# Kernel optimization log

Hardware: AMD Instinct MI355X
Metric: run time of the kernel (lower is better)

The kernel has to match this reference:

```python
import jax, jax.numpy as jnp
import numpy as np

B, GH, GW = 8, 32, 32
S = GH * GW            # 1024
HIDDEN = 512
D = 64                 # head_dim
NUM_HOPS = 2
EPS = 1e-6


def setup_inputs() -> dict:
    key = jax.random.key(0)
    ks = jax.random.split(key, 8)

    def init(k, shape, std):
        return (jax.random.normal(k, shape) * std).astype(jnp.float32)

    x = jax.random.normal(ks[0], (B, S, HIDDEN), dtype=jnp.float32)
    Wq = init(ks[1], (D, HIDDEN), HIDDEN ** -0.5)
    Wk = init(ks[2], (D, HIDDEN), HIDDEN ** -0.5)
    Wv = init(ks[3], (D, HIDDEN), HIDDEN ** -0.5)
    bias_table = init(ks[4], (2 * GH - 1, 2 * GW - 1), 0.02)
    fusion_w = jnp.ones((NUM_HOPS, 3), dtype=jnp.float32)
    fusion_b = jnp.zeros((NUM_HOPS,), dtype=jnp.float32)
    hop_W = init(ks[5], (NUM_HOPS, D, D), D ** -0.5)
    gate_W = init(ks[6], (NUM_HOPS, HIDDEN), HIDDEN ** -0.5)
    gate_b = jnp.zeros((NUM_HOPS,), dtype=jnp.float32)
    out_W = init(ks[7], (HIDDEN, D), D ** -0.5)
    temperature = jnp.ones((1,), dtype=jnp.float32)

    # relative position index [S, S] (buffer, constant)
    coords = np.stack(np.meshgrid(np.arange(GH), np.arange(GW), indexing='ij')).reshape(2, -1)
    rel = coords[:, :, None] - coords[:, None, :]
    rel[0] += GH - 1
    rel[1] += GW - 1
    rel_idx = jnp.asarray(rel[0] * (2 * GW - 1) + rel[1], dtype=jnp.int32)

    return dict(x=x, Wq=Wq, Wk=Wk, Wv=Wv, bias_table=bias_table,
                fusion_w=fusion_w, fusion_b=fusion_b, hop_W=hop_W,
                gate_W=gate_W, gate_b=gate_b, out_W=out_W,
                temperature=temperature, rel_idx=rel_idx)


def _rotate_half(u):
    d = u.shape[-1] // 2
    return jnp.concatenate([-u[..., d:], u[..., :d]], axis=-1)


def _prob_log(p):
    p = jnp.clip(p, EPS, 1.0 - EPS)
    return jnp.log(p / (1.0 - p + EPS))


def _mat_exp(M, h):
    R = M
    for _ in range(h - 1):
        R = jnp.matmul(R, M)
    return R


def _row_norm(M):
    return M / (jnp.sum(M, axis=-1, keepdims=True) + EPS)


def reference(x, Wq, Wk, Wv, bias_table, fusion_w, fusion_b, hop_W,
              gate_W, gate_b, out_W, temperature, rel_idx):
    b, s, hdim = x.shape
    d = Wq.shape[0]
    n_hops = hop_W.shape[0]
    scale = jnp.sqrt(jnp.float32(d))

    Q = jnp.einsum('bsh,dh->bsd', x, Wq)
    K = jnp.einsum('bsh,dh->bsd', x, Wk)
    V = jnp.einsum('bsh,dh->bsd', x, Wv)

    # RoPE (cached cos/sin are deterministic functions of S, D)
    inv_freq = 1.0 / (10000.0 ** (jnp.arange(0, d, 2, dtype=jnp.float32) / d))
    t = jnp.arange(s, dtype=jnp.float32)
    emb = jnp.concatenate([jnp.outer(t, inv_freq)] * 2, axis=-1)  # [S, D]
    cos, sin = jnp.cos(emb), jnp.sin(emb)
    Q = Q * cos + _rotate_half(Q) * sin
    K = K * cos + _rotate_half(K) * sin

    pb = bias_table.reshape(-1)[rel_idx]  # [S, S]
    scores = (jnp.einsum('bsd,btd->bst', Q, K) / scale + pb[None])
    scores = scores / jnp.clip(temperature, 0.1, None)
    A = jax.nn.softmax(scores, axis=-1)  # [B, S, S]

    A_T = jnp.swapaxes(A, -1, -2)
    AAt = jnp.matmul(A, A_T)
    AtA = jnp.matmul(A_T, A)

    hop_outs = []
    for hop in range(n_hops):
        h = hop + 1
        A_seq = _row_norm(_mat_exp(A, h))
        A_co = _row_norm(_mat_exp(AAt, h))
        A_sp = _row_norm(_mat_exp(AtA, h))
        fused_logit = (fusion_b[hop]
                       + fusion_w[hop, 0] * _prob_log(A_seq)
                       + fusion_w[hop, 1] * _prob_log(A_co)
                       + fusion_w[hop, 2] * _prob_log(A_sp))
        fused = _row_norm(jax.nn.sigmoid(fused_logit))
        hop_v = jnp.einsum('bsd,ed->bse', V, hop_W[hop])
        hop_outs.append(jnp.matmul(fused, hop_v))  # [B, S, D]

    gate = jax.nn.softmax(jnp.einsum('bsh,gh->bsg', x, gate_W) + gate_b, axis=-1)
    combined = sum(hop_outs[i] * gate[..., i:i + 1] for i in range(n_hops))
    return jnp.einsum('bsd,hd->bsh', combined, out_W)
```

## Files before the change

### kernel.cpp

```cpp
#include <hip/hip_runtime.h>
#include <hip/hip_bf16.h>

#define BB 8
#define SS 1024
#define HH 512
#define DD 64

typedef unsigned short u16;
typedef short v8s __attribute__((ext_vector_type(8)));
typedef float v4f __attribute__((ext_vector_type(4)));

__device__ __forceinline__ float bf2f(u16 u) {
    union { unsigned int i; float f; } v; v.i = ((unsigned int)u) << 16; return v.f;
}
__device__ __forceinline__ u16 f2bf(float f) {
    union { float f; unsigned int i; } v; v.f = f;
    unsigned int u = v.i;
    unsigned int r = u + 0x7fffu + ((u >> 16) & 1u);
    return (u16)(r >> 16);
}

__device__ __forceinline__ void gload16(const u16* g, u16* l) {
    __builtin_amdgcn_global_load_lds(
        (const __attribute__((address_space(1))) void*)g,
        (__attribute__((address_space(3))) void*)l,
        16, 0, 0);
}

__device__ __forceinline__ void tile_1024(
    const u16* __restrict__ Xb, const u16* __restrict__ Yb,
    u16* __restrict__ Cd, int tm, int tn, u16* Xs, u16* Ys, int mirror)
{
    int t = threadIdx.x, lane = t & 63, w = t >> 6;
    int wm = (w & 1) << 6, wn = (w >> 1) << 6;
    int fr = lane & 15, q = lane >> 4, m7 = fr & 7;
    int subrow = lane >> 3, cch = (lane & 7) ^ subrow;

    const u16* xg[4]; const u16* yg[4]; u16* xl[4]; u16* yl[4];
    #pragma unroll
    for (int i = 0; i < 4; i++) {
        int r = i * 32 + w * 8 + subrow;
        xg[i] = Xb + (long)(tm + r) * 1024 + cch * 8;
        yg[i] = Yb + (long)(tn + r) * 1024 + cch * 8;
        xl[i] = Xs + (i * 32 + w * 8) * 64;
        yl[i] = Ys + (i * 32 + w * 8) * 64;
    }

    v4f acc[4][4];
    #pragma unroll
    for (int i = 0; i < 4; i++)
        #pragma unroll
        for (int j = 0; j < 4; j++) {
            acc[i][j][0] = 0.f; acc[i][j][1] = 0.f; acc[i][j][2] = 0.f; acc[i][j][3] = 0.f;
        }

    for (int k0 = 0; k0 < 1024; k0 += 64) {
        __syncthreads();
        #pragma unroll
        for (int i = 0; i < 4; i++) { gload16(xg[i] + k0, xl[i]); gload16(yg[i] + k0, yl[i]); }
        __syncthreads();
        v8s af[2][4], bfr[2][4];
        #pragma unroll
        for (int h = 0; h < 2; h++) {
            int ca = (((h << 2) + q) ^ m7) << 3;
            #pragma unroll
            for (int s = 0; s < 4; s++) {
                af[h][s]  = *(const v8s*)(Xs + (wm + s * 16 + fr) * 64 + ca);
                bfr[h][s] = *(const v8s*)(Ys + (wn + s * 16 + fr) * 64 + ca);
            }
        }
        #pragma unroll
        for (int h = 0; h < 2; h++)
            #pragma unroll
            for (int i = 0; i < 4; i++)
                #pragma unroll
                for (int j = 0; j < 4; j++)
                    acc[i][j] = __builtin_amdgcn_mfma_f32_16x16x32_bf16(af[h][i], bfr[h][j], acc[i][j], 0, 0, 0);
    }
    #pragma unroll
    for (int i = 0; i < 4; i++) {
        int rowb = tm + wm + i * 16 + q * 4;
        #pragma unroll
        for (int j = 0; j < 4; j++) {
            int col = tn + wn + j * 16 + fr;
            ushort4 pv;
            pv.x = f2bf(acc[i][j][0]); pv.y = f2bf(acc[i][j][1]);
            pv.z = f2bf(acc[i][j][2]); pv.w = f2bf(acc[i][j][3]);
            #pragma unroll
            for (int r = 0; r < 4; r++)
                Cd[(long)(rowb + r) * 1024 + col] = ((u16*)&pv)[r];
            if (mirror)
                *(ushort4*)(Cd + (long)col * 1024 + rowb) = pv;
        }
    }
}

__device__ __forceinline__ void hopv_tile(
    const u16* __restrict__ Vrows, const u16* __restrict__ Hw,
    u16* __restrict__ hopVT, int tm, u16* Xs, u16* Ys)
{
    int t = threadIdx.x, lane = t & 63, w = t >> 6;
    int wm = (w & 1) << 6, wn = (w >> 1) << 6;
    int fr = lane & 15, q = lane >> 4, m7 = fr & 7;
    int subrow = lane >> 3, cch = (lane & 7) ^ subrow;

    #pragma unroll
    for (int i = 0; i < 4; i++) {
        int r = i * 32 + w * 8 + subrow;
        gload16(Vrows + (long)(tm + r) * 64 + cch * 8, Xs + (i * 32 + w * 8) * 64);
        gload16(Hw + (long)r * 64 + cch * 8, Ys + (i * 32 + w * 8) * 64);
    }
    __syncthreads();

    v4f acc[4][4];
    #pragma unroll
    for (int i = 0; i < 4; i++)
        #pragma unroll
        for (int j = 0; j < 4; j++) {
            acc[i][j][0] = 0.f; acc[i][j][1] = 0.f; acc[i][j][2] = 0.f; acc[i][j][3] = 0.f;
        }
    v8s af[2][4], bfr[2][4];
    #pragma unroll
    for (int h = 0; h < 2; h++) {
        int ca = (((h << 2) + q) ^ m7) << 3;
        #pragma unroll
        for (int s = 0; s < 4; s++) {
            af[h][s]  = *(const v8s*)(Xs + (wm + s * 16 + fr) * 64 + ca);
            bfr[h][s] = *(const v8s*)(Ys + (wn + s * 16 + fr) * 64 + ca);
        }
    }
    #pragma unroll
    for (int h = 0; h < 2; h++)
        #pragma unroll
        for (int i = 0; i < 4; i++)
            #pragma unroll
            for (int j = 0; j < 4; j++)
                acc[i][j] = __builtin_amdgcn_mfma_f32_16x16x32_bf16(af[h][i], bfr[h][j], acc[i][j], 0, 0, 0);

    int z = tm >> 10, sb = tm & 1023;
    #pragma unroll
    for (int i = 0; i < 4; i++) {
        int rowb = wm + i * 16 + q * 4;
        #pragma unroll
        for (int j = 0; j < 4; j++) {
            int colY = wn + j * 16 + fr;
            int hop = colY >> 6, e = colY & 63;
            ushort4 pv;
            pv.x = f2bf(acc[i][j][0]); pv.y = f2bf(acc[i][j][1]);
            pv.z = f2bf(acc[i][j][2]); pv.w = f2bf(acc[i][j][3]);
            *(ushort4*)(hopVT + (long)(hop * 8 + z) * 65536 + (long)e * 1024 + sb + rowb) = pv;
        }
    }
}

__device__ __forceinline__ void hop_tile(
    const u16* __restrict__ Fb, const u16* __restrict__ Hb,
    int y, int tmt, float* __restrict__ Pd, u16* Fs, u16* Hs)
{
    int tm = tmt * 128, kb = y * 256;
    int t = threadIdx.x, lane = t & 63, w = t >> 6;
    int fr = lane & 15, q = lane >> 4, m7 = fr & 7;
    int subrow = lane >> 3, cch = (lane & 7) ^ subrow;

    const u16* fg[4]; u16* fl[4]; const u16* hg[2]; u16* hl[2];
    #pragma unroll
    for (int i = 0; i < 4; i++) {
        int r = i * 32 + w * 8 + subrow;
        fg[i] = Fb + (long)(tm + r) * 1024 + cch * 8;
        fl[i] = Fs + (i * 32 + w * 8) * 64;
    }
    #pragma unroll
    for (int i = 0; i < 2; i++) {
        int r = i * 32 + w * 8 + subrow;
        hg[i] = Hb + (long)r * 1024 + cch * 8;
        hl[i] = Hs + (i * 32 + w * 8) * 64;
    }

    v4f acc[2][4];
    #pragma unroll
    for (int i = 0; i < 2; i++)
        #pragma unroll
        for (int j = 0; j < 4; j++) {
            acc[i][j][0] = 0.f; acc[i][j][1] = 0.f; acc[i][j][2] = 0.f; acc[i][j][3] = 0.f;
        }

    for (int k0 = kb; k0 < kb + 256; k0 += 64) {
        __syncthreads();
        #pragma unroll
        for (int i = 0; i < 4; i++) gload16(fg[i] + k0, fl[i]);
        #pragma unroll
        for (int i = 0; i < 2; i++) gload16(hg[i] + k0, hl[i]);
        __syncthreads();
        v8s af[2][2], bfr[2][4];
        #pragma unroll
        for (int h = 0; h < 2; h++) {
            int ca = (((h << 2) + q) ^ m7) << 3;
            #pragma unroll
            for (int s = 0; s < 2; s++)
                af[h][s] = *(const v8s*)(Fs + (w * 32 + s * 16 + fr) * 64 + ca);
            #pragma unroll
            for (int s = 0; s < 4; s++)
                bfr[h][s] = *(const v8s*)(Hs + (s * 16 + fr) * 64 + ca);
        }
        #pragma unroll
        for (int h = 0; h < 2; h++)
            #pragma unroll
            for (int i = 0; i < 2; i++)
                #pragma unroll
                for (int j = 0; j < 4; j++)
                    acc[i][j] = __builtin_amdgcn_mfma_f32_16x16x32_bf16(af[h][i], bfr[h][j], acc[i][j], 0, 0, 0);
    }
    #pragma unroll
    for (int i = 0; i < 2; i++) {
        int rowb = tm + w * 32 + i * 16 + q * 4;
        #pragma unroll
        for (int j = 0; j < 4; j++) {
            int col = j * 16 + fr;
            #pragma unroll
            for (int r = 0; r < 4; r++)
                Pd[(long)(rowb + r) * 64 + col] = acc[i][j][r];
        }
    }
}

__device__ __forceinline__ void fused_row(
    const u16* __restrict__ r1, const u16* __restrict__ r2, const u16* __restrict__ r3,
    float w0, float w1, float w2, float b0, u16* __restrict__ Frow, int lane)
{
    int base = lane << 4;
    union U { uint4 v; u16 s[8]; };
    U a[2], b[2], c[2];
    a[0].v = *(const uint4*)(r1 + base); a[1].v = *(const uint4*)(r1 + base + 8);
    b[0].v = *(const uint4*)(r2 + base); b[1].v = *(const uint4*)(r2 + base + 8);
    c[0].v = *(const uint4*)(r3 + base); c[1].v = *(const uint4*)(r3 + base + 8);
    float m1[16], m2[16], m3[16];
    float s1 = 0.f, s2 = 0.f, s3 = 0.f;
    #pragma unroll
    for (int h = 0; h < 2; h++)
        #pragma unroll
        for (int e = 0; e < 8; e++) {
            int k = h * 8 + e;
            m1[k] = bf2f(a[h].s[e]); m2[k] = bf2f(b[h].s[e]); m3[k] = bf2f(c[h].s[e]);
            s1 += m1[k]; s2 += m2[k]; s3 += m3[k];
        }
    #pragma unroll
    for (int o = 1; o < 64; o <<= 1) {
        s1 += __shfl_xor(s1, o); s2 += __shfl_xor(s2, o); s3 += __shfl_xor(s3, o);
    }
    float i1 = 1.f / (s1 + 1e-6f), i2 = 1.f / (s2 + 1e-6f), i3 = 1.f / (s3 + 1e-6f);
    float sig[16];
    float ssum = 0.f;
    #pragma unroll
    for (int k = 0; k < 16; k++) {
        float p1 = fminf(fmaxf(m1[k] * i1, 1e-6f), 1.0f - 1e-6f);
        float p2 = fminf(fmaxf(m2[k] * i2, 1e-6f), 1.0f - 1e-6f);
        float p3 = fminf(fmaxf(m3[k] * i3, 1e-6f), 1.0f - 1e-6f);
        float l1 = __logf(p1 / (1.0f - p1 + 1e-6f));
        float l2 = __logf(p2 / (1.0f - p2 + 1e-6f));
        float l3 = __logf(p3 / (1.0f - p3 + 1e-6f));
        float lg = b0 + w0 * l1 + w1 * l2 + w2 * l3;
        float sg = 1.0f / (1.0f + __expf(-lg));
        sig[k] = sg; ssum += sg;
    }
    #pragma unroll
    for (int o = 1; o < 64; o <<= 1) ssum += __shfl_xor(ssum, o);
    float inv = 1.0f / (ssum + 1e-6f);
    U o0, o1;
    #pragma unroll
    for (int e = 0; e < 8; e++) { o0.s[e] = f2bf(sig[e] * inv); o1.s[e] = f2bf(sig[8 + e] * inv); }
    *(uint4*)(Frow + base) = o0.v;
    *(uint4*)(Frow + base + 8) = o1.v;
}

__global__ __launch_bounds__(256) void k_qksm(
    const u16* __restrict__ Qb, const u16* __restrict__ Kb,
    const float* __restrict__ btab, const float* __restrict__ temp,
    u16* __restrict__ A, u16* __restrict__ AT)
{
    __shared__ __align__(16) float smf[3969];
    __shared__ float lred[4][16];
    int t = threadIdx.x, lane = t & 63, w = t >> 6;
    int fr = lane & 15, q4 = lane >> 4;
    int bx = blockIdx.x;
    int z = bx >> 6;
    int rb = (bx & 63) << 4;
    for (int i = t; i < 3969; i += 256) smf[i] = btab[i];
    __syncthreads();
    float invt = 1.0f / fmaxf(temp[0], 0.1f);
    const long SD = (long)SS * DD;
    const long SSq = (long)SS * SS;
    const u16* qrow = Qb + (long)z * SD + (long)(rb + fr) * 64 + q4 * 8;
    v8s aq0 = *(const v8s*)(qrow);
    v8s aq1 = *(const v8s*)(qrow + 32);
    int ih[4], iw[4];
    #pragma unroll
    for (int r = 0; r < 4; r++) {
        int ii = rb + q4 * 4 + r;
        ih[r] = ii >> 5; iw[r] = ii & 31;
    }
    const u16* kb0 = Kb + (long)z * SD + q4 * 8;
    int c0 = w << 8;
    float ef[16][4];
    float l0 = 0.f, l1 = 0.f, l2 = 0.f, l3 = 0.f;
    #pragma unroll
    for (int f = 0; f < 16; f++) {
        int colK = c0 + f * 16 + fr;
        const u16* krow = kb0 + (long)colK * 64;
        v8s bk0 = *(const v8s*)(krow);
        v8s bk1 = *(const v8s*)(krow + 32);
        v4f acc = {0.f, 0.f, 0.f, 0.f};
        acc = __builtin_amdgcn_mfma_f32_16x16x32_bf16(aq0, bk0, acc, 0, 0, 0);
        acc = __builtin_amdgcn_mfma_f32_16x16x32_bf16(aq1, bk1, acc, 0, 0, 0);
        int jh = colK >> 5, jw = colK & 31;
        #pragma unroll
        for (int r = 0; r < 4; r++) {
            float pb = smf[(ih[r] - jh + 31) * 63 + (iw[r] - jw + 31)];
            float s = (acc[r] * 0.125f + pb) * invt;
            float e = __expf(s);
            ef[f][r] = e;
            if (r == 0) l0 += e; else if (r == 1) l1 += e;
            else if (r == 2) l2 += e; else l3 += e;
        }
    }
    #pragma unroll
    for (int o = 1; o < 16; o <<= 1) {
        l0 += __shfl_xor(l0, o); l1 += __shfl_xor(l1, o);
        l2 += __shfl_xor(l2, o); l3 += __shfl_xor(l3, o);
    }
    if (fr == 0) {
        lred[w][q4 * 4 + 0] = l0; lred[w][q4 * 4 + 1] = l1;
        lred[w][q4 * 4 + 2] = l2; lred[w][q4 * 4 + 3] = l3;
    }
    __syncthreads();
    float invl[4];
    #pragma unroll
    for (int r = 0; r < 4; r++) {
        int idx = q4 * 4 + r;
        invl[r] = 1.0f / (lred[0][idx] + lred[1][idx] + lred[2][idx] + lred[3][idx]);
    }
    u16* Ab = A + (long)z * SSq;
    u16* ATb = AT + (long)z * SSq;
    #pragma unroll
    for (int f = 0; f < 16; f++) {
        int colK = c0 + f * 16 + fr;
        ushort4 pv;
        u16* pp = (u16*)&pv;
        #pragma unroll
        for (int r = 0; r < 4; r++) {
            u16 bv = f2bf(ef[f][r] * invl[r]);
            pp[r] = bv;
            Ab[(long)(rb + q4 * 4 + r) * 1024 + colK] = bv;
        }
        *(ushort4*)(ATb + (long)colK * 1024 + rb + q4 * 4) = pv;
    }
}

__global__ __launch_bounds__(256) void gemm_link1(
    const u16* __restrict__ A, const u16* __restrict__ AT,
    u16* __restrict__ AAt, u16* __restrict__ AtA, u16* __restrict__ A2,
    const u16* __restrict__ Vb, const u16* __restrict__ hopWb,
    u16* __restrict__ hopVT)
{
    __shared__ u16 Xs[128 * 64];
    __shared__ u16 Ys[128 * 64];
    const long SSq = (long)SS * SS;
    if (blockIdx.x >= 1088) {
        hopv_tile(Vb, hopWb, hopVT, (blockIdx.x - 1088) * 128, Xs, Ys);
        return;
    }
    int b = blockIdx.x & 7;
    int job = blockIdx.x >> 3;
    const u16* Xb; const u16* Yb; u16* Cd;
    int ti, tj, mir;
    if (job < 72) {
        int tt = job < 36 ? job : job - 36;
        ti = 0;
        while (tt >= 8 - ti) { tt -= 8 - ti; ti++; }
        tj = ti + tt;
        mir = (ti != tj);
        if (job < 36) { Xb = A  + b * SSq; Yb = Xb; Cd = AAt + b * SSq; }
        else          { Xb = AT + b * SSq; Yb = Xb; Cd = AtA + b * SSq; }
    } else {
        int jj = job - 72;
        ti = jj >> 3; tj = jj & 7; mir = 0;
        Xb = A + b * SSq; Yb = AT + b * SSq; Cd = A2 + b * SSq;
    }
    tile_1024(Xb, Yb, Cd, ti * 128, tj * 128, Xs, Ys, mir);
}

__global__ __launch_bounds__(256) void k_link2_fused0(
    const u16* __restrict__ AAt, const u16* __restrict__ AtA,
    u16* __restrict__ AAt2, u16* __restrict__ AtA2,
    const u16* __restrict__ A, const float* __restrict__ fw,
    const float* __restrict__ fbv, u16* __restrict__ F0)
{
    __shared__ u16 Xs[128 * 64];
    __shared__ u16 Ys[128 * 64];
    const long SSq = (long)SS * SS;
    int bx = blockIdx.x;
    if (bx < 576) {
        int z = bx & 15;
        int tt = bx >> 4, ti = 0;
        while (tt >= 8 - ti) { tt -= 8 - ti; ti++; }
        int tj = ti + tt;
        const u16* Xb = (z < 8 ? AAt : AtA) + (long)(z & 7) * SSq;
        u16* Cd = (z < 8 ? AAt2 : AtA2) + (long)(z & 7) * SSq;
        tile_1024(Xb, Xb, Cd, ti * 128, tj * 128, Xs, Ys, ti != tj);
    } else {
        int lane = threadIdx.x & 63, w = threadIdx.x >> 6;
        float w0 = fw[0], w1 = fw[1], w2 = fw[2], b0 = fbv[0];
        long row = (long)(bx - 576) * 4 + w;
        fused_row(A + row * 1024, AAt + row * 1024, AtA + row * 1024,
                  w0, w1, w2, b0, F0 + row * 1024, lane);
    }
}

__global__ __launch_bounds__(256) void k_hop0_fused1(
    const u16* __restrict__ F0, const u16* __restrict__ hopVT,
    float* __restrict__ Pa, float* __restrict__ Pb,
    const u16* __restrict__ A2, const u16* __restrict__ AAt2,
    const u16* __restrict__ AtA2, const float* __restrict__ fw,
    const float* __restrict__ fbv, u16* __restrict__ F1)
{
    __shared__ u16 Fs[128 * 64];
    __shared__ u16 Hs[64 * 64];
    const long SSq = (long)SS * SS;
    int bx = blockIdx.x;
    if (bx < 256) {
        int y = bx >> 6, rest = bx & 63;
        int tmt = rest >> 3, b = rest & 7;
        float* Pd = (y < 2 ? Pa + (long)y * 16 * 65536 : Pb + (long)(y - 2) * 16 * 65536)
                    + (long)b * 65536;
        hop_tile(F0 + (long)b * SSq, hopVT + (long)b * 65536, y, tmt, Pd, Fs, Hs);
    } else {
        int lane = threadIdx.x & 63, w = threadIdx.x >> 6;
        float w0 = fw[3], w1 = fw[4], w2 = fw[5], b0 = fbv[1];
        long row = (long)(bx - 256) * 4 + w;
        fused_row(A2 + row * 1024, AAt2 + row * 1024, AtA2 + row * 1024,
                  w0, w1, w2, b0, F1 + row * 1024, lane);
    }
}

__global__ __launch_bounds__(256) void gemm_hop1(
    const u16* __restrict__ F1, const u16* __restrict__ hopVT,
    float* __restrict__ Pa, float* __restrict__ Pb)
{
    __shared__ u16 Fs[128 * 64];
    __shared__ u16 Hs[64 * 64];
    const long SSq = (long)SS * SS;
    int j = blockIdx.x;
    int y = j >> 6, rest = j & 63;
    int tmt = rest >> 3, b = rest & 7;
    float* Pd = (y < 2 ? Pa + (long)y * 16 * 65536 : Pb + (long)(y - 2) * 16 * 65536)
                + (long)(8 + b) * 65536;
    hop_tile(F1 + (long)b * SSq, hopVT + (long)(8 + b) * 65536, y, tmt, Pd, Fs, Hs);
}

__global__ __launch_bounds__(256) void gemm_nt(
    const u16* __restrict__ X, long sx,
    const u16* __restrict__ Y, long sy,
    void* __restrict__ Cv, long sc,
    int M, int N, int K, int cf32)
{
    __shared__ u16 Xs[128 * 64];
    __shared__ u16 Ys[128 * 64];
    const u16* Xb = X + (long)blockIdx.z * sx;
    const u16* Yb = Y + (long)blockIdx.z * sy;
    int tm = blockIdx.x * 128, tn = blockIdx.y * 128;
    int t = threadIdx.x, lane = t & 63, w = t >> 6;
    int wm = (w & 1) << 6, wn = (w >> 1) << 6;
    int fr = lane & 15, q = lane >> 4, m7 = fr & 7;
    int subrow = lane >> 3, cch = (lane & 7) ^ subrow;

    const u16* xg[4]; const u16* yg[4]; u16* xl[4]; u16* yl[4];
    #pragma unroll
    for (int i = 0; i < 4; i++) {
        int r = i * 32 + w * 8 + subrow;
        xg[i] = Xb + (long)(tm + r) * K + cch * 8;
        yg[i] = Yb + (long)(tn + r) * K + cch * 8;
        xl[i] = Xs + (i * 32 + w * 8) * 64;
        yl[i] = Ys + (i * 32 + w * 8) * 64;
    }

    v4f acc[4][4];
    #pragma unroll
    for (int i = 0; i < 4; i++)
        #pragma unroll
        for (int j = 0; j < 4; j++) {
            acc[i][j][0] = 0.f; acc[i][j][1] = 0.f; acc[i][j][2] = 0.f; acc[i][j][3] = 0.f;
        }

    for (int k0 = 0; k0 < K; k0 += 64) {
        __syncthreads();
        #pragma unroll
        for (int i = 0; i < 4; i++) { gload16(xg[i] + k0, xl[i]); gload16(yg[i] + k0, yl[i]); }
        __syncthreads();
        v8s af[2][4], bfr[2][4];
        #pragma unroll
        for (int h = 0; h < 2; h++) {
            int ca = (((h << 2) + q) ^ m7) << 3;
            #pragma unroll
            for (int s = 0; s < 4; s++) {
                af[h][s]  = *(const v8s*)(Xs + (wm + s * 16 + fr) * 64 + ca);
                bfr[h][s] = *(const v8s*)(Ys + (wn + s * 16 + fr) * 64 + ca);
            }
        }
        #pragma unroll
        for (int h = 0; h < 2; h++)
            #pragma unroll
            for (int i = 0; i < 4; i++)
                #pragma unroll
                for (int j = 0; j < 4; j++)
                    acc[i][j] = __builtin_amdgcn_mfma_f32_16x16x32_bf16(af[h][i], bfr[h][j], acc[i][j], 0, 0, 0);
    }
    long cb = (long)blockIdx.z * sc;
    #pragma unroll
    for (int i = 0; i < 4; i++) {
        int rowb = tm + wm + i * 16 + q * 4;
        #pragma unroll
        for (int j = 0; j < 4; j++) {
            int col = tn + wn + j * 16 + fr;
            #pragma unroll
            for (int r = 0; r < 4; r++) {
                long o = cb + (long)(rowb + r) * N + col;
                if (cf32) ((float*)Cv)[o] = acc[i][j][r];
                else      ((u16*)Cv)[o] = f2bf(acc[i][j][r]);
            }
        }
    }
}

__global__ __launch_bounds__(256) void k_proj_rope(
    const u16* __restrict__ xb, const u16* __restrict__ wpack,
    const float* __restrict__ gateb, const float2* __restrict__ ropetab,
    u16* __restrict__ Qb, u16* __restrict__ Kb, u16* __restrict__ Vb,
    float* __restrict__ gate)
{
    __shared__ u16 Xs[128 * 64];
    __shared__ u16 Ys[128 * 64];
    int tm = blockIdx.x * 128, tn = blockIdx.y * 128;
    int t = threadIdx.x, lane = t & 63, w = t >> 6;
    int wm = (w & 1) << 6, wn = (w >> 1) << 6;
    int fr = lane & 15, q = lane >> 4, m7 = fr & 7;
    int subrow = lane >> 3, cch = (lane & 7) ^ subrow;

    const u16* xg[4]; const u16* yg[4]; u16* xl[4]; u16* yl[4];
    #pragma unroll
    for (int i = 0; i < 4; i++) {
        int r = i * 32 + w * 8 + subrow;
        xg[i] = xb + (long)(tm + r) * 512 + cch * 8;
        yg[i] = wpack + (long)(tn + r) * 512 + cch * 8;
        xl[i] = Xs + (i * 32 + w * 8) * 64;
        yl[i] = Ys + (i * 32 + w * 8) * 64;
    }

    v4f acc[4][4];
    #pragma unroll
    for (int i = 0; i < 4; i++)
        #pragma unroll
        for (int j = 0; j < 4; j++) {
            acc[i][j][0] = 0.f; acc[i][j][1] = 0.f; acc[i][j][2] = 0.f; acc[i][j][3] = 0.f;
        }

    for (int k0 = 0; k0 < 512; k0 += 64) {
        __syncthreads();
        #pragma unroll
        for (int i = 0; i < 4; i++) { gload16(xg[i] + k0, xl[i]); gload16(yg[i] + k0, yl[i]); }
        __syncthreads();
        v8s af[2][4], bfr[2][4];
        #pragma unroll
        for (int h = 0; h < 2; h++) {
            int ca = (((h << 2) + q) ^ m7) << 3;
            #pragma unroll
            for (int s = 0; s < 4; s++) {
                af[h][s]  = *(const v8s*)(Xs + (wm + s * 16 + fr) * 64 + ca);
                bfr[h][s] = *(const v8s*)(Ys + (wn + s * 16 + fr) * 64 + ca);
            }
        }
        #pragma unroll
        for (int h = 0; h < 2; h++)
            #pragma unroll
            for (int i = 0; i < 4; i++)
                #pragma unroll
                for (int j = 0; j < 4; j++)
                    acc[i][j] = __builtin_amdgcn_mfma_f32_16x16x32_bf16(af[h][i], bfr[h][j], acc[i][j], 0, 0, 0);
    }

    if (blockIdx.y == 0) {
        u16* dst = wn ? Kb : Qb;
        #pragma unroll
        for (int i = 0; i < 4; i++) {
            #pragma unroll
            for (int r = 0; r < 4; r++) {
                int row = tm + wm + i * 16 + q * 4 + r;
                int spos = row & (SS - 1);
                float2 t0 = ropetab[spos * 32 + fr];
                float2 t1 = ropetab[spos * 32 + 16 + fr];
                #pragma unroll
                for (int j = 0; j < 4; j++) {
                    float v = acc[i][j][r], p = acc[i][j ^ 2][r];
                    float cs = (j & 1) ? t1.x : t0.x;
                    float sn = (j & 1) ? t1.y : t0.y;
                    float o = (j & 2) ? (v * cs + p * sn) : (v * cs - p * sn);
                    dst[(long)row * 64 + j * 16 + fr] = f2bf(o);
                }
            }
        }
    } else if (wn == 0) {
        #pragma unroll
        for (int i = 0; i < 4; i++)
            #pragma unroll
            for (int j = 0; j < 4; j++)
                #pragma unroll
                for (int r = 0; r < 4; r++) {
                    int row = tm + wm + i * 16 + q * 4 + r;
                    Vb[(long)row * 64 + j * 16 + fr] = f2bf(acc[i][j][r]);
                }
    } else {
        float gb = gateb[fr & 1];
        #pragma unroll
        for (int i = 0; i < 4; i++)
            #pragma unroll
            for (int r = 0; r < 4; r++) {
                int row = tm + wm + i * 16 + q * 4 + r;
                float g = acc[i][0][r] + gb;
                float go = __shfl_xor(g, 1);
                float m = fmaxf(g, go);
                float e = __expf(g - m), eo = __expf(go - m);
                if (fr < 2) gate[(long)row * 2 + fr] = e / (e + eo);
            }
    }
}

__global__ __launch_bounds__(256) void k_pack(
    const float* __restrict__ x, const float* __restrict__ Wq,
    const float* __restrict__ Wk, const float* __restrict__ Wv,
    const float* __restrict__ gW, const float* __restrict__ hopW,
    const float* __restrict__ outW, u16* __restrict__ xb,
    u16* __restrict__ wpack, u16* __restrict__ hopWb, u16* __restrict__ outWb,
    float2* __restrict__ ropetab)
{
    int bx = blockIdx.x;
    if (bx < 4096) {
        long i = (long)bx * 256 + threadIdx.x;
        float4 v = ((const float4*)x)[i];
        ushort4 o;
        o.x = f2bf(v.x); o.y = f2bf(v.y); o.z = f2bf(v.z); o.w = f2bf(v.w);
        ((ushort4*)xb)[i] = o;
    } else if (bx < 4768) {
        int idx = (bx - 4096) * 256 + threadIdx.x;
        if (idx < 131072) {
            int r = idx >> 9, c = idx & 511;
            float v = 0.f;
            if (r < 64)       v = Wq[r * 512 + c];
            else if (r < 128) v = Wk[(r - 64) * 512 + c];
            else if (r < 192) v = Wv[(r - 128) * 512 + c];
            else if (r < 194) v = gW[(r - 192) * 512 + c];
            wpack[idx] = f2bf(v);
        } else if (idx < 131072 + 8192) {
            int i = idx - 131072;
            hopWb[i] = f2bf(hopW[i]);
        } else if (idx < 131072 + 8192 + 32768) {
            int i = idx - 131072 - 8192;
            outWb[i] = f2bf(outW[i]);
        }
    } else {
        int idx = (bx - 4768) * 256 + threadIdx.x;
        int spos = idx >> 5, f = idx & 31;
        float ang = (float)spos * exp2f(-(float)f * (13.287712379549449f / 32.0f));
        float sn, cs;
        sincosf(ang, &sn, &cs);
        ropetab[idx] = make_float2(cs, sn);
    }
}

__global__ __launch_bounds__(256) void k_combine(
    const float* __restrict__ Pa, const float* __restrict__ Pb,
    const float* __restrict__ gate, u16* __restrict__ comb)
{
    long idx = (long)blockIdx.x * 256 + threadIdx.x;
    long srow = idx >> 6;
    int b = (int)(srow >> 10);
    long o = (long)(srow & 1023) * 64 + (idx & 63);
    float h0 = Pa[(long)b * 65536 + o] + Pa[(long)(16 + b) * 65536 + o]
             + Pb[(long)b * 65536 + o] + Pb[(long)(16 + b) * 65536 + o];
    float h1 = Pa[(long)(8 + b) * 65536 + o] + Pa[(long)(24 + b) * 65536 + o]
             + Pb[(long)(8 + b) * 65536 + o] + Pb[(long)(24 + b) * 65536 + o];
    float g0 = gate[srow * 2], g1 = gate[srow * 2 + 1];
    comb[idx] = f2bf(h0 * g0 + h1 * g1);
}

extern "C" void kernel_launch(void* const* d_in, const int* in_sizes, int n_in,
                              void* d_out, int out_size, void* d_ws, size_t ws_size,
                              hipStream_t stream) {
    const float* x    = (const float*)d_in[0];
    const float* Wq   = (const float*)d_in[1];
    const float* Wk   = (const float*)d_in[2];
    const float* Wv   = (const float*)d_in[3];
    const float* btab = (const float*)d_in[4];
    const float* fw   = (const float*)d_in[5];
    const float* fbv  = (const float*)d_in[6];
    const float* hopW = (const float*)d_in[7];
    const float* gW   = (const float*)d_in[8];
    const float* gb   = (const float*)d_in[9];
    const float* outW = (const float*)d_in[10];
    const float* temp = (const float*)d_in[11];
    float* out = (float*)d_out;

    char* wsb = (char*)d_ws;
    size_t off = 0;
    auto take = [&](size_t n) { char* p = wsb + off; off += (n + 255) & ~(size_t)255; return p; };
    u16* Qb      = (u16*)take(8192L * 64 * 2);
    u16* Kb      = (u16*)take(8192L * 64 * 2);
    u16* Vb      = (u16*)take(8192L * 64 * 2);
    float* gate  = (float*)take(8192L * 2 * 4);
    u16* wpack   = (u16*)take(256L * 512 * 2);
    u16* hopWb   = (u16*)take(2L * 64 * 64 * 2);
    u16* outWb   = (u16*)take(512L * 64 * 2);
    float2* ropetab = (float2*)take(1024L * 32 * 8);
    u16* hopVT   = (u16*)take(2L * 8 * 64 * 1024 * 2);
    float* Pa    = (float*)take(2L * 16 * 65536 * 4);
    u16* comb    = (u16*)take(8192L * 64 * 2);
    char* fregion = take(8L * 1024 * 1024 * 4);
    u16* F0      = (u16*)fregion;
    u16* F1      = (u16*)fregion + 8L * 1024 * 1024;
    u16* A       = (u16*)take(8L * 1024 * 1024 * 2);
    u16* xb      = (u16*)A;
    u16* AT      = (u16*)take(8L * 1024 * 1024 * 2);
    float* Pb    = (float*)AT;
    u16* AAt     = (u16*)take(8L * 1024 * 1024 * 2);
    u16* AtA     = (u16*)take(8L * 1024 * 1024 * 2);
    u16* A2      = (u16*)take(8L * 1024 * 1024 * 2);
    u16* AAt2    = (u16*)take(8L * 1024 * 1024 * 2);
    u16* AtA2    = (u16*)take(8L * 1024 * 1024 * 2);
    (void)ws_size; (void)in_sizes; (void)n_in; (void)out_size;

    k_pack<<<4896, 256, 0, stream>>>(x, Wq, Wk, Wv, gW, hopW, outW, xb, wpack,
                                     hopWb, outWb, ropetab);
    k_proj_rope<<<dim3(64, 2, 1), 256, 0, stream>>>(xb, wpack, gb, ropetab,
                                                    Qb, Kb, Vb, gate);
    k_qksm<<<512, 256, 0, stream>>>(Qb, Kb, btab, temp, A, AT);
    gemm_link1<<<1152, 256, 0, stream>>>(A, AT, AAt, AtA, A2, Vb, hopWb, hopVT);
    k_link2_fused0<<<2624, 256, 0, stream>>>(AAt, AtA, AAt2, AtA2, A, fw, fbv, F0);
    k_hop0_fused1<<<2304, 256, 0, stream>>>(F0, hopVT, Pa, Pb, A2, AAt2, AtA2,
                                            fw, fbv, F1);
    gemm_hop1<<<256, 256, 0, stream>>>(F1, hopVT, Pa, Pb);
    k_combine<<<2048, 256, 0, stream>>>(Pa, Pb, gate, comb);
    gemm_nt<<<dim3(64, 4, 1), 256, 0, stream>>>(comb, 0, outWb, 0, out, 0, 8192, 512, 64, 1);
}
```

Baseline: 276.8 us.

## Fuse x bf16 conversion into projection and move hop-V tiles into softmax kernel

Drops the separate fp32-to-bf16 pass over x in k_pack; the projection kernel now loads fp32 x directly and converts while writing to LDS. The projection launch becomes one 512-thread block per row tile covering all 256 output columns, so x is read once instead of twice. The hop-V tiles move from gemm_link1 into k_qksm as extra blocks, reusing its shared buffer, so they overlap with the lighter softmax kernel. The risks are a less efficient x load path (plain register loads instead of direct global-to-LDS) and only 64 blocks in the projection kernel.

```diff
diff --git a/kernel.cpp b/kernel.cpp
--- a/kernel.cpp
+++ b/kernel.cpp
@@ -275,13 +275,20 @@
 __global__ __launch_bounds__(256) void k_qksm(
     const u16* __restrict__ Qb, const u16* __restrict__ Kb,
     const float* __restrict__ btab, const float* __restrict__ temp,
-    u16* __restrict__ A, u16* __restrict__ AT)
-{
-    __shared__ __align__(16) float smf[3969];
+    u16* __restrict__ A, u16* __restrict__ AT,
+    const u16* __restrict__ Vb, const u16* __restrict__ hopWb,
+    u16* __restrict__ hopVT)
+{
+    __shared__ __align__(16) u16 sbuf[2][128 * 64];
     __shared__ float lred[4][16];
     int t = threadIdx.x, lane = t & 63, w = t >> 6;
+    int bx = blockIdx.x;
+    if (bx >= 512) {
+        hopv_tile(Vb, hopWb, hopVT, (bx - 512) * 128, sbuf[0], sbuf[1]);
+        return;
+    }
+    float* smf = (float*)sbuf;
     int fr = lane & 15, q4 = lane >> 4;
-    int bx = blockIdx.x;
     int z = bx >> 6;
     int rb = (bx & 63) << 4;
     for (int i = t; i < 3969; i += 256) smf[i] = btab[i];
@@ -357,17 +364,11 @@
 
 __global__ __launch_bounds__(256) void gemm_link1(
     const u16* __restrict__ A, const u16* __restrict__ AT,
-    u16* __restrict__ AAt, u16* __restrict__ AtA, u16* __restrict__ A2,
-    const u16* __restrict__ Vb, const u16* __restrict__ hopWb,
-    u16* __restrict__ hopVT)
+    u16* __restrict__ AAt, u16* __restrict__ AtA, u16* __restrict__ A2)
 {
     __shared__ u16 Xs[128 * 64];
     __shared__ u16 Ys[128 * 64];
     const long SSq = (long)SS * SS;
-    if (blockIdx.x >= 1088) {
-        hopv_tile(Vb, hopWb, hopVT, (blockIdx.x - 1088) * 128, Xs, Ys);
-        return;
-    }
     int b = blockIdx.x & 7;
     int job = blockIdx.x >> 3;
     const u16* Xb; const u16* Yb; u16* Cd;
@@ -530,28 +531,33 @@
     }
 }
 
-__global__ __launch_bounds__(256) void k_proj_rope(
-    const u16* __restrict__ xb, const u16* __restrict__ wpack,
+__global__ __launch_bounds__(512) void k_proj_rope(
+    const float* __restrict__ x, const u16* __restrict__ wpack,
     const float* __restrict__ gateb, const float2* __restrict__ ropetab,
     u16* __restrict__ Qb, u16* __restrict__ Kb, u16* __restrict__ Vb,
     float* __restrict__ gate)
 {
     __shared__ u16 Xs[128 * 64];
-    __shared__ u16 Ys[128 * 64];
-    int tm = blockIdx.x * 128, tn = blockIdx.y * 128;
+    __shared__ u16 Ys[256 * 64];
+    int tm = blockIdx.x * 128;
     int t = threadIdx.x, lane = t & 63, w = t >> 6;
     int wm = (w & 1) << 6, wn = (w >> 1) << 6;
     int fr = lane & 15, q = lane >> 4, m7 = fr & 7;
     int subrow = lane >> 3, cch = (lane & 7) ^ subrow;
 
-    const u16* xg[4]; const u16* yg[4]; u16* xl[4]; u16* yl[4];
+    const u16* yg[4]; u16* yl[4];
     #pragma unroll
     for (int i = 0; i < 4; i++) {
-        int r = i * 32 + w * 8 + subrow;
-        xg[i] = xb + (long)(tm + r) * 512 + cch * 8;
-        yg[i] = wpack + (long)(tn + r) * 512 + cch * 8;
-        xl[i] = Xs + (i * 32 + w * 8) * 64;
-        yl[i] = Ys + (i * 32 + w * 8) * 64;
+        int r = i * 64 + w * 8 + subrow;
+        yg[i] = wpack + (long)r * 512 + cch * 8;
+        yl[i] = Ys + (i * 64 + w * 8) * 64;
+    }
+    const float* xg[2]; u16* xw[2];
+    #pragma unroll
+    for (int i = 0; i < 2; i++) {
+        int r = i * 64 + w * 8 + subrow;
+        xg[i] = x + (long)(tm + r) * 512 + cch * 8;
+        xw[i] = Xs + r * 64 + (lane & 7) * 8;
     }
 
     v4f acc[4][4];
@@ -565,7 +571,18 @@
     for (int k0 = 0; k0 < 512; k0 += 64) {
         __syncthreads();
         #pragma unroll
-        for (int i = 0; i < 4; i++) { gload16(xg[i] + k0, xl[i]); gload16(yg[i] + k0, yl[i]); }
+        for (int i = 0; i < 4; i++) gload16(yg[i] + k0, yl[i]);
+        #pragma unroll
+        for (int i = 0; i < 2; i++) {
+            float4 v0 = *(const float4*)(xg[i] + k0);
+            float4 v1 = *(const float4*)(xg[i] + k0 + 4);
+            v8s pk;
+            pk[0] = (short)f2bf(v0.x); pk[1] = (short)f2bf(v0.y);
+            pk[2] = (short)f2bf(v0.z); pk[3] = (short)f2bf(v0.w);
+            pk[4] = (short)f2bf(v1.x); pk[5] = (short)f2bf(v1.y);
+            pk[6] = (short)f2bf(v1.z); pk[7] = (short)f2bf(v1.w);
+            *(v8s*)xw[i] = pk;
+        }
         __syncthreads();
         v8s af[2][4], bfr[2][4];
         #pragma unroll
@@ -586,7 +603,7 @@
                     acc[i][j] = __builtin_amdgcn_mfma_f32_16x16x32_bf16(af[h][i], bfr[h][j], acc[i][j], 0, 0, 0);
     }
 
-    if (blockIdx.y == 0) {
+    if (wn < 128) {
         u16* dst = wn ? Kb : Qb;
         #pragma unroll
         for (int i = 0; i < 4; i++) {
@@ -606,7 +623,7 @@
                 }
             }
         }
-    } else if (wn == 0) {
+    } else if (wn == 128) {
         #pragma unroll
         for (int i = 0; i < 4; i++)
             #pragma unroll
@@ -633,22 +650,15 @@
 }
 
 __global__ __launch_bounds__(256) void k_pack(
-    const float* __restrict__ x, const float* __restrict__ Wq,
-    const float* __restrict__ Wk, const float* __restrict__ Wv,
-    const float* __restrict__ gW, const float* __restrict__ hopW,
-    const float* __restrict__ outW, u16* __restrict__ xb,
+    const float* __restrict__ Wq, const float* __restrict__ Wk,
+    const float* __restrict__ Wv, const float* __restrict__ gW,
+    const float* __restrict__ hopW, const float* __restrict__ outW,
     u16* __restrict__ wpack, u16* __restrict__ hopWb, u16* __restrict__ outWb,
     float2* __restrict__ ropetab)
 {
     int bx = blockIdx.x;
-    if (bx < 4096) {
-        long i = (long)bx * 256 + threadIdx.x;
-        float4 v = ((const float4*)x)[i];
-        ushort4 o;
-        o.x = f2bf(v.x); o.y = f2bf(v.y); o.z = f2bf(v.z); o.w = f2bf(v.w);
-        ((ushort4*)xb)[i] = o;
-    } else if (bx < 4768) {
-        int idx = (bx - 4096) * 256 + threadIdx.x;
+    if (bx < 672) {
+        int idx = bx * 256 + threadIdx.x;
         if (idx < 131072) {
             int r = idx >> 9, c = idx & 511;
             float v = 0.f;
@@ -665,7 +675,7 @@
             outWb[i] = f2bf(outW[i]);
         }
     } else {
-        int idx = (bx - 4768) * 256 + threadIdx.x;
+        int idx = (bx - 672) * 256 + threadIdx.x;
         int spos = idx >> 5, f = idx & 31;
         float ang = (float)spos * exp2f(-(float)f * (13.287712379549449f / 32.0f));
         float sn, cs;
@@ -725,7 +735,6 @@
     u16* F0      = (u16*)fregion;
     u16* F1      = (u16*)fregion + 8L * 1024 * 1024;
     u16* A       = (u16*)take(8L * 1024 * 1024 * 2);
-    u16* xb      = (u16*)A;
     u16* AT      = (u16*)take(8L * 1024 * 1024 * 2);
     float* Pb    = (float*)AT;
     u16* AAt     = (u16*)take(8L * 1024 * 1024 * 2);
@@ -735,12 +744,12 @@
     u16* AtA2    = (u16*)take(8L * 1024 * 1024 * 2);
     (void)ws_size; (void)in_sizes; (void)n_in; (void)out_size;
 
-    k_pack<<<4896, 256, 0, stream>>>(x, Wq, Wk, Wv, gW, hopW, outW, xb, wpack,
-                                     hopWb, outWb, ropetab);
-    k_proj_rope<<<dim3(64, 2, 1), 256, 0, stream>>>(xb, wpack, gb, ropetab,
-                                                    Qb, Kb, Vb, gate);
-    k_qksm<<<512, 256, 0, stream>>>(Qb, Kb, btab, temp, A, AT);
-    gemm_link1<<<1152, 256, 0, stream>>>(A, AT, AAt, AtA, A2, Vb, hopWb, hopVT);
+    k_pack<<<800, 256, 0, stream>>>(Wq, Wk, Wv, gW, hopW, outW, wpack,
+                                    hopWb, outWb, ropetab);
+    k_proj_rope<<<64, 512, 0, stream>>>(x, wpack, gb, ropetab,
+                                        Qb, Kb, Vb, gate);
+    k_qksm<<<576, 256, 0, stream>>>(Qb, Kb, btab, temp, A, AT, Vb, hopWb, hopVT);
+    gemm_link1<<<1088, 256, 0, stream>>>(A, AT, AAt, AtA, A2);
     k_link2_fused0<<<2624, 256, 0, stream>>>(AAt, AtA, AAt2, AtA2, A, fw, fbv, F0);
     k_hop0_fused1<<<2304, 256, 0, stream>>>(F0, hopVT, Pa, Pb, A2, AAt2, AtA2,
                                             fw, fbv, F1);
```

After: 287.3 us. 3.8% more time.
